# Kernel tuning notes

Hardware: AMD Instinct MI355X
Metric: run time of the kernel (lower is better)

Reference implementation:

```python
import jax, jax.numpy as jnp
import numpy as np

B, S, D, H, E, K, DH = 4, 2048, 1024, 8, 8, 2, 128
ROPE_BASE = 10000.0


def setup_inputs() -> dict:
    key = jax.random.key(0)
    ks = jax.random.split(key, 7)
    s = 1.0 / np.sqrt(D)
    x = jax.random.normal(ks[0], (B, S, D), dtype=jnp.float32)
    Wq = jax.random.normal(ks[1], (H * DH, D), dtype=jnp.float32) * s
    Wk = jax.random.normal(ks[2], (H * DH, D), dtype=jnp.float32) * s
    Wv = jax.random.normal(ks[3], (H * E, D, DH), dtype=jnp.float32) * s
    Wo = jax.random.normal(ks[4], (H * E, DH, D), dtype=jnp.float32) * (1.0 / np.sqrt(H * DH))
    sel_v = jax.random.normal(ks[5], (H * E, D), dtype=jnp.float32) * s
    sel_o = jax.random.normal(ks[6], (H * E, D), dtype=jnp.float32) * s
    positions = jnp.broadcast_to(jnp.arange(S, dtype=jnp.int32), (B, S))
    return {"x": x, "Wq": Wq, "Wk": Wk, "Wv": Wv, "Wo": Wo,
            "sel_v": sel_v, "sel_o": sel_o, "positions": positions}


def _rope(t, pos, inv_freq):
    # t: [b,h,s,d], pos: [b,s]
    freqs = pos.astype(t.dtype)[:, :, None] * inv_freq          # [b,s,d/2]
    emb = jnp.concatenate([freqs, freqs], axis=-1)[:, None]      # [b,1,s,d]
    sin, cos = jnp.sin(emb), jnp.cos(emb)
    x1, x2 = jnp.split(t, 2, axis=-1)
    rot = jnp.concatenate([-x2, x1], axis=-1)
    return t * cos + rot * sin


def reference(x, Wq, Wk, Wv, Wo, sel_v, sel_o, positions):
    # dense shared Q/K projections -> [b,h,s,dh]
    q = (x @ Wq.T).reshape(B, S, H, DH).transpose(0, 2, 1, 3)
    k = (x @ Wk.T).reshape(B, S, H, DH).transpose(0, 2, 1, 3)

    # V expert routing (sigmoid, non-competitive top-k per head)
    gv = jax.nn.sigmoid((x @ sel_v.T).reshape(B, S, H, E))       # [b,s,h,e]
    vw, vi = jax.lax.top_k(gv, K)                                # [b,s,h,k]
    vall = jnp.einsum('bsm,hemd->bshed', x, Wv.reshape(H, E, D, DH))
    vsel = jnp.take_along_axis(vall, vi[..., None], axis=3)      # [b,s,h,k,dh]
    v = (vw[..., None] * vsel).sum(axis=3).transpose(0, 2, 1, 3)  # [b,h,s,dh]

    # RoPE (rotate_fraction=1 -> full head dim)
    inv_freq = 1.0 / (ROPE_BASE ** (jnp.arange(0, DH, 2, dtype=jnp.float32) / DH))
    q = _rope(q, positions, inv_freq)
    k = _rope(k, positions, inv_freq)

    # masked SDPA (causal bool mask, scale 1/sqrt(dh))
    scores = jnp.einsum('bhqd,bhkd->bhqk', q, k) * (1.0 / np.sqrt(DH))
    causal = jnp.tril(jnp.ones((S, S), dtype=bool))
    scores = jnp.where(causal, scores, jnp.finfo(scores.dtype).min)
    attn = jax.nn.softmax(scores, axis=-1)
    ctx = jnp.einsum('bhqk,bhkd->bqhd', attn, v)                  # [b,s,h,dh]

    # O expert routing, combine via scattered gate weights
    go = jax.nn.sigmoid((x @ sel_o.T).reshape(B, S, H, E))
    ow, oi = jax.lax.top_k(go, K)
    g_full = (ow[..., None] * jax.nn.one_hot(oi, E, dtype=x.dtype)).sum(axis=3)  # [b,s,h,e]
    out = jnp.einsum('bshd,bshe,hedm->bsm', ctx, g_full, Wo.reshape(H, E, DH, D))
    return out
```

## Files before the change

### kernel.cpp

```cpp
#include <hip/hip_runtime.h>
#include <math.h>

typedef unsigned short u16;
typedef unsigned int u32;
typedef __attribute__((ext_vector_type(8))) short short8;
typedef __attribute__((ext_vector_type(4))) float f32x4;

constexpr int cB = 4, cS = 2048, cD = 1024, cH = 8, cE = 8, cK = 2, cDH = 128;
constexpr int cBS = cB * cS;
constexpr int cHE = cH * cE;

__device__ inline u16 f2bf(float f) {
    u32 u = __float_as_uint(f);
    u += 0x7fffu + ((u >> 16) & 1u);
    return (u16)(u >> 16);
}
__device__ inline float bf2f(u16 h) { return __uint_as_float(((u32)h) << 16); }

__global__ __launch_bounds__(256) void k_cast_split(
    const float* __restrict__ src, u16* __restrict__ hi, u16* __restrict__ lo)
{
    const size_t i = (size_t)blockIdx.x * 256 + threadIdx.x;
    float4 v = ((const float4*)src)[i];
    u16 hx = f2bf(v.x), hy = f2bf(v.y), hz = f2bf(v.z), hw = f2bf(v.w);
    u16 lx = f2bf(v.x - bf2f(hx)), ly = f2bf(v.y - bf2f(hy));
    u16 lz = f2bf(v.z - bf2f(hz)), lw = f2bf(v.w - bf2f(hw));
    uint2 oh; oh.x = (u32)hx | ((u32)hy << 16); oh.y = (u32)hz | ((u32)hw << 16);
    uint2 ol; ol.x = (u32)lx | ((u32)ly << 16); ol.y = (u32)lz | ((u32)lw << 16);
    ((uint2*)hi)[i] = oh;
    ((uint2*)lo)[i] = ol;
}

__global__ __launch_bounds__(256, 2) void k_gemm_logits3(
    const u16* __restrict__ xh, const u16* __restrict__ xlo,
    const u16* __restrict__ selh, const u16* __restrict__ sell,
    float* __restrict__ lgp)
{
    __shared__ u16 As[128 * 72];
    __shared__ u16 Bs[128 * 72];
    const int r0 = blockIdx.x * 128;
    const int term = blockIdx.y;
    const u16* A = (term == 1) ? xlo : xh;
    const u16* B = (term == 2) ? sell : selh;
    float* outp = lgp + (size_t)term * cBS * 128;
    const int t = threadIdx.x;
    const int w = t >> 6, lane = t & 63;
    const int wm = w >> 1, wn = w & 1;
    const int quad = lane >> 4, lm = lane & 15;

    f32x4 acc[4][4];
#pragma unroll
    for (int i = 0; i < 4; i++)
#pragma unroll
        for (int j = 0; j < 4; j++)
#pragma unroll
            for (int r = 0; r < 4; r++) acc[i][j][r] = 0.0f;

    for (int kc = 0; kc < cD; kc += 64) {
#pragma unroll
        for (int p = 0; p < 4; p++) {
            const int slot = p * 256 + t, row = slot >> 3, seg = slot & 7;
            *(uint4*)(As + row * 72 + seg * 8) =
                *(const uint4*)(A + (size_t)(r0 + row) * cD + kc + seg * 8);
            *(uint4*)(Bs + row * 72 + seg * 8) =
                *(const uint4*)(B + (size_t)row * cD + kc + seg * 8);
        }
        __syncthreads();
#pragma unroll
        for (int ks = 0; ks < 64; ks += 32) {
            short8 av[4], bv[4];
#pragma unroll
            for (int i = 0; i < 4; i++)
                av[i] = *(const short8*)(As + (wm * 64 + i * 16 + lm) * 72 + ks + quad * 8);
#pragma unroll
            for (int j = 0; j < 4; j++)
                bv[j] = *(const short8*)(Bs + (wn * 64 + j * 16 + lm) * 72 + ks + quad * 8);
#pragma unroll
            for (int i = 0; i < 4; i++)
#pragma unroll
                for (int j = 0; j < 4; j++)
                    acc[i][j] = __builtin_amdgcn_mfma_f32_16x16x32_bf16(av[i], bv[j], acc[i][j], 0, 0, 0);
        }
        __syncthreads();
    }
#pragma unroll
    for (int i = 0; i < 4; i++)
#pragma unroll
        for (int r = 0; r < 4; r++) {
            const int row = r0 + wm * 64 + i * 16 + quad * 4 + r;
#pragma unroll
            for (int j = 0; j < 4; j++)
                outp[(size_t)row * 128 + wn * 64 + j * 16 + lm] = acc[i][j][r];
        }
}

__global__ __launch_bounds__(256) void k_top2_flag(
    const float* __restrict__ lgp, float* __restrict__ gv_d, float* __restrict__ go_d,
    int* __restrict__ flags, int* __restrict__ counter)
{
    const int idx = blockIdx.x * 256 + threadIdx.x;
    const int row = idx >> 4, r16 = idx & 15;
    const int which = r16 >> 3, h = r16 & 7;
    const float* l0 = lgp + (size_t)row * 128 + which * 64 + h * 8;
    const float* l1 = l0 + (size_t)cBS * 128;
    const float* l2 = l1 + (size_t)cBS * 128;
    float v[8];
#pragma unroll
    for (int e = 0; e < cE; e++) v[e] = l0[e] + l1[e] + l2[e];
    int i0 = 0; float b0 = v[0];
#pragma unroll
    for (int e = 1; e < cE; e++) { if (v[e] > b0) { b0 = v[e]; i0 = e; } }
    int i1 = -1; float b1 = -3.0e38f;
#pragma unroll
    for (int e = 0; e < cE; e++) { if (e != i0 && v[e] > b1) { b1 = v[e]; i1 = e; } }
    float b2 = -3.0e38f;
#pragma unroll
    for (int e = 0; e < cE; e++) { if (e != i0 && e != i1 && v[e] > b2) b2 = v[e]; }
    const float w0 = 1.0f / (1.0f + __expf(-b0));
    const float w1 = 1.0f / (1.0f + __expf(-b1));
    float* dst = (which ? go_d : gv_d) + (size_t)row * 64 + h * 8;
#pragma unroll
    for (int e = 0; e < cE; e++)
        dst[e] = (e == i0) ? w0 : ((e == i1) ? w1 : 0.0f);
    if (b1 - b2 < 1.0e-3f) {
        const int s = atomicAdd(counter, 1);
        flags[s] = (row << 4) | r16;
    }
}

__global__ __launch_bounds__(64) void k_repair(
    const float* __restrict__ x, const float* __restrict__ sel_v,
    const float* __restrict__ sel_o,
    const int* __restrict__ counter, const int* __restrict__ flags,
    float* __restrict__ gv_d, float* __restrict__ go_d)
{
    const int n = *counter;
    const int lane = threadIdx.x;
    for (int it = blockIdx.x; it < n; it += gridDim.x) {
        const int item = flags[it];
        const int row = item >> 4, which = (item >> 3) & 1, h = item & 7;
        const float* xr = x + (size_t)row * cD;
        const float* sb = (which ? sel_o : sel_v) + (size_t)(h * 8) * cD;
        float lg[8];
#pragma unroll
        for (int e = 0; e < cE; e++) {
            float a = 0.0f;
#pragma unroll
            for (int dg = 0; dg < 4; dg++) {
                const int d = dg * 256 + lane * 4;
                const float4 xv = *(const float4*)(xr + d);
                const float4 sv = *(const float4*)(sb + (size_t)e * cD + d);
                a += xv.x * sv.x + xv.y * sv.y + xv.z * sv.z + xv.w * sv.w;
            }
#pragma unroll
            for (int off = 1; off < 64; off <<= 1) a += __shfl_xor(a, off);
            lg[e] = a;
        }
        int i0 = 0; float b0 = lg[0];
#pragma unroll
        for (int e = 1; e < cE; e++) { if (lg[e] > b0) { b0 = lg[e]; i0 = e; } }
        int i1 = -1; float b1 = -3.0e38f;
#pragma unroll
        for (int e = 0; e < cE; e++) { if (e != i0 && lg[e] > b1) { b1 = lg[e]; i1 = e; } }
        if (lane == 0) {
            const float w0 = 1.0f / (1.0f + expf(-b0));
            const float w1 = 1.0f / (1.0f + expf(-b1));
            float* dst = (which ? go_d : gv_d) + (size_t)row * 64 + h * 8;
#pragma unroll
            for (int e = 0; e < cE; e++)
                dst[e] = (e == i0) ? w0 : ((e == i1) ? w1 : 0.0f);
        }
    }
}

__global__ __launch_bounds__(256) void k_cast_f2b(
    const float* __restrict__ src, u16* __restrict__ dst)
{
    const size_t i = (size_t)blockIdx.x * 256 + threadIdx.x;
    float4 v = ((const float4*)src)[i];
    u32 lo = (u32)f2bf(v.x) | ((u32)f2bf(v.y) << 16);
    u32 hi = (u32)f2bf(v.z) | ((u32)f2bf(v.w) << 16);
    uint2 o; o.x = lo; o.y = hi;
    ((uint2*)dst)[i] = o;
}

__global__ __launch_bounds__(256) void k_cast_wv(
    const float* __restrict__ Wv, u16* __restrict__ WvT)
{
    __shared__ float ld[64][132];
    const int d0 = blockIdx.x * 64, he = blockIdx.y;
    const int t = threadIdx.x;
    for (int p = 0; p < 8; p++) {
        const int slot = p * 256 + t, r = slot >> 5, c4 = slot & 31;
        float4 v = *(const float4*)(Wv + ((size_t)he * cD + d0 + r) * cDH + c4 * 4);
        ld[r][c4 * 4 + 0] = v.x; ld[r][c4 * 4 + 1] = v.y;
        ld[r][c4 * 4 + 2] = v.z; ld[r][c4 * 4 + 3] = v.w;
    }
    __syncthreads();
    for (int p = 0; p < 16; p++) {
        const int slot = p * 256 + t, dh = slot >> 5, c2 = slot & 31;
        u32 val = (u32)f2bf(ld[c2 * 2 + 0][dh]) | ((u32)f2bf(ld[c2 * 2 + 1][dh]) << 16);
        *(u32*)(WvT + (size_t)(he * cDH + dh) * cD + d0 + c2 * 2) = val;
    }
}

__global__ __launch_bounds__(256) void k_cast_wo(
    const float* __restrict__ Wo, u16* __restrict__ WoT)
{
    __shared__ float ld[128][68];
    const int m0 = blockIdx.x * 64, he = blockIdx.y;
    const int t = threadIdx.x;
    for (int p = 0; p < 8; p++) {
        const int slot = p * 256 + t, r = slot >> 4, c4 = slot & 15;
        float4 v = *(const float4*)(Wo + ((size_t)he * cDH + r) * cD + m0 + c4 * 4);
        ld[r][c4 * 4 + 0] = v.x; ld[r][c4 * 4 + 1] = v.y;
        ld[r][c4 * 4 + 2] = v.z; ld[r][c4 * 4 + 3] = v.w;
    }
    __syncthreads();
    for (int p = 0; p < 16; p++) {
        const int slot = p * 256 + t, mr = slot >> 6, c2 = slot & 63;
        u32 val = (u32)f2bf(ld[c2 * 2 + 0][mr]) | ((u32)f2bf(ld[c2 * 2 + 1][mr]) << 16);
        *(u32*)(WoT + (size_t)(m0 + mr) * 8192 + he * cDH + c2 * 2) = val;
    }
}

__global__ __launch_bounds__(256, 2) void k_gemm_v(
    const u16* __restrict__ xh, const u16* __restrict__ WvT,
    const float* __restrict__ gv_d, u16* __restrict__ v_b)
{
    __shared__ u16 As[128 * 72];
    __shared__ u16 Bs[128 * 72];
    __shared__ float Gs[128][9];
    const int rt = blockIdx.x, h = blockIdx.y;
    const int r0 = rt * 128;
    const int t = threadIdx.x;
    const int w = t >> 6, lane = t & 63;
    const int wm = w >> 1, wn = w & 1;
    const int quad = lane >> 4, lm = lane & 15;

    {
        const int row = t >> 1, half = t & 1;
        float4 g4 = *(const float4*)(gv_d + (size_t)(r0 + row) * 64 + h * 8 + half * 4);
        Gs[row][half * 4 + 0] = g4.x; Gs[row][half * 4 + 1] = g4.y;
        Gs[row][half * 4 + 2] = g4.z; Gs[row][half * 4 + 3] = g4.w;
    }

    f32x4 acc[4][4];
#pragma unroll
    for (int i = 0; i < 4; i++)
#pragma unroll
        for (int j = 0; j < 4; j++)
#pragma unroll
            for (int r = 0; r < 4; r++) acc[i][j][r] = 0.0f;

    for (int e = 0; e < cE; e++) {
        f32x4 acce[4][4];
#pragma unroll
        for (int i = 0; i < 4; i++)
#pragma unroll
            for (int j = 0; j < 4; j++)
#pragma unroll
                for (int r = 0; r < 4; r++) acce[i][j][r] = 0.0f;

        for (int kc = 0; kc < cD; kc += 64) {
#pragma unroll
            for (int p = 0; p < 4; p++) {
                const int slot = p * 256 + t, row = slot >> 3, seg = slot & 7;
                *(uint4*)(As + row * 72 + seg * 8) =
                    *(const uint4*)(xh + (size_t)(r0 + row) * cD + kc + seg * 8);
                *(uint4*)(Bs + row * 72 + seg * 8) =
                    *(const uint4*)(WvT + (size_t)((h * 8 + e) * cDH + row) * cD + kc + seg * 8);
            }
            __syncthreads();
#pragma unroll
            for (int ks = 0; ks < 64; ks += 32) {
                short8 av[4], bv[4];
#pragma unroll
                for (int i = 0; i < 4; i++)
                    av[i] = *(const short8*)(As + (wm * 64 + i * 16 + lm) * 72 + ks + quad * 8);
#pragma unroll
                for (int j = 0; j < 4; j++)
                    bv[j] = *(const short8*)(Bs + (wn * 64 + j * 16 + lm) * 72 + ks + quad * 8);
#pragma unroll
                for (int i = 0; i < 4; i++)
#pragma unroll
                    for (int j = 0; j < 4; j++)
                        acce[i][j] = __builtin_amdgcn_mfma_f32_16x16x32_bf16(av[i], bv[j], acce[i][j], 0, 0, 0);
            }
            __syncthreads();
        }
#pragma unroll
        for (int i = 0; i < 4; i++)
#pragma unroll
            for (int r = 0; r < 4; r++) {
                const float g = Gs[wm * 64 + i * 16 + quad * 4 + r][e];
#pragma unroll
                for (int j = 0; j < 4; j++) acc[i][j][r] += g * acce[i][j][r];
            }
    }
#pragma unroll
    for (int i = 0; i < 4; i++)
#pragma unroll
        for (int r = 0; r < 4; r++) {
            const int row = r0 + wm * 64 + i * 16 + quad * 4 + r;
            const int b = row >> 11, s = row & (cS - 1);
            u16* dst = v_b + ((size_t)(b * cH + h) * cS + s) * cDH;
#pragma unroll
            for (int j = 0; j < 4; j++)
                dst[wn * 64 + j * 16 + lm] = f2bf(acc[i][j][r]);
        }
}

__global__ __launch_bounds__(256, 2) void k_gemm_o(
    const u16* __restrict__ ctxh, const u16* __restrict__ WoT,
    const float* __restrict__ go_d, float* __restrict__ out)
{
    __shared__ u16 As[128 * 72];
    __shared__ u16 Bs[128 * 72];
    __shared__ float Gs[128][65];
    const int rt = blockIdx.x, nt = blockIdx.y;
    const int r0 = rt * 128;
    const int t = threadIdx.x;
    const int w = t >> 6, lane = t & 63;
    const int wm = w >> 1, wn = w & 1;
    const int quad = lane >> 4, lm = lane & 15;

#pragma unroll
    for (int p = 0; p < 8; p++) {
        const int slot = p * 256 + t, row = slot >> 4, seg = slot & 15;
        float4 g4 = *(const float4*)(go_d + (size_t)(r0 + row) * 64 + seg * 4);
        Gs[row][seg * 4 + 0] = g4.x; Gs[row][seg * 4 + 1] = g4.y;
        Gs[row][seg * 4 + 2] = g4.z; Gs[row][seg * 4 + 3] = g4.w;
    }

    f32x4 acc[4][4];
#pragma unroll
    for (int i = 0; i < 4; i++)
#pragma unroll
        for (int j = 0; j < 4; j++)
#pragma unroll
            for (int r = 0; r < 4; r++) acc[i][j][r] = 0.0f;

    for (int he = 0; he < cHE; he++) {
        f32x4 acce[4][4];
#pragma unroll
        for (int i = 0; i < 4; i++)
#pragma unroll
            for (int j = 0; j < 4; j++)
#pragma unroll
                for (int r = 0; r < 4; r++) acce[i][j][r] = 0.0f;

#pragma unroll
        for (int kc = 0; kc < 2; kc++) {
            const int ccol = (he >> 3) * 128 + kc * 64;
#pragma unroll
            for (int p = 0; p < 4; p++) {
                const int slot = p * 256 + t, row = slot >> 3, seg = slot & 7;
                *(uint4*)(As + row * 72 + seg * 8) =
                    *(const uint4*)(ctxh + (size_t)(r0 + row) * cD + ccol + seg * 8);
                *(uint4*)(Bs + row * 72 + seg * 8) =
                    *(const uint4*)(WoT + (size_t)(nt * 128 + row) * 8192 + he * 128 + kc * 64 + seg * 8);
            }
            __syncthreads();
#pragma unroll
            for (int ks = 0; ks < 64; ks += 32) {
                short8 av[4], bv[4];
#pragma unroll
                for (int i = 0; i < 4; i++)
                    av[i] = *(const short8*)(As + (wm * 64 + i * 16 + lm) * 72 + ks + quad * 8);
#pragma unroll
                for (int j = 0; j < 4; j++)
                    bv[j] = *(const short8*)(Bs + (wn * 64 + j * 16 + lm) * 72 + ks + quad * 8);
#pragma unroll
                for (int i = 0; i < 4; i++)
#pragma unroll
                    for (int j = 0; j < 4; j++)
                        acce[i][j] = __builtin_amdgcn_mfma_f32_16x16x32_bf16(av[i], bv[j], acce[i][j], 0, 0, 0);
            }
            __syncthreads();
        }
#pragma unroll
        for (int i = 0; i < 4; i++)
#pragma unroll
            for (int r = 0; r < 4; r++) {
                const float g = Gs[wm * 64 + i * 16 + quad * 4 + r][he];
#pragma unroll
                for (int j = 0; j < 4; j++) acc[i][j][r] += g * acce[i][j][r];
            }
    }
#pragma unroll
    for (int i = 0; i < 4; i++)
#pragma unroll
        for (int r = 0; r < 4; r++) {
            const int row = r0 + wm * 64 + i * 16 + quad * 4 + r;
            float* dst = out + (size_t)row * cD + nt * 128;
#pragma unroll
            for (int j = 0; j < 4; j++)
                dst[wn * 64 + j * 16 + lm] = acc[i][j][r];
        }
}

__global__ __launch_bounds__(256, 2) void k_qkproj_mfma(
    const u16* __restrict__ xh, const u16* __restrict__ Wqb,
    const u16* __restrict__ Wkb, float* __restrict__ q_t, float* __restrict__ k_t)
{
    __shared__ u16 As[128 * 72];
    __shared__ u16 Bs[128 * 72];
    const int rt = blockIdx.x, nt = blockIdx.y;
    const bool isK = nt >= cH;
    const int h = isK ? nt - cH : nt;
    const u16* Wb = isK ? Wkb : Wqb;
    float* outp = isK ? k_t : q_t;
    const int r0 = rt * 128;
    const int t = threadIdx.x;
    const int w = t >> 6, lane = t & 63;
    const int wm = w >> 1, wn = w & 1;
    const int quad = lane >> 4, lm = lane & 15;

    f32x4 acc[4][4];
#pragma unroll
    for (int i = 0; i < 4; i++)
#pragma unroll
        for (int j = 0; j < 4; j++)
#pragma unroll
            for (int r = 0; r < 4; r++) acc[i][j][r] = 0.0f;

    for (int kc = 0; kc < cD; kc += 64) {
#pragma unroll
        for (int p = 0; p < 4; p++) {
            const int slot = p * 256 + t, row = slot >> 3, seg = slot & 7;
            *(uint4*)(As + row * 72 + seg * 8) =
                *(const uint4*)(xh + (size_t)(r0 + row) * cD + kc + seg * 8);
            *(uint4*)(Bs + row * 72 + seg * 8) =
                *(const uint4*)(Wb + (size_t)(h * cDH + row) * cD + kc + seg * 8);
        }
        __syncthreads();
#pragma unroll
        for (int ks = 0; ks < 64; ks += 32) {
            short8 av[4], bv[4];
#pragma unroll
            for (int i = 0; i < 4; i++)
                av[i] = *(const short8*)(As + (wm * 64 + i * 16 + lm) * 72 + ks + quad * 8);
#pragma unroll
            for (int j = 0; j < 4; j++)
                bv[j] = *(const short8*)(Bs + (wn * 64 + j * 16 + lm) * 72 + ks + quad * 8);
#pragma unroll
            for (int i = 0; i < 4; i++)
#pragma unroll
                for (int j = 0; j < 4; j++)
                    acc[i][j] = __builtin_amdgcn_mfma_f32_16x16x32_bf16(av[i], bv[j], acc[i][j], 0, 0, 0);
        }
        __syncthreads();
    }
#pragma unroll
    for (int i = 0; i < 4; i++)
#pragma unroll
        for (int r = 0; r < 4; r++) {
            const int row = r0 + wm * 64 + i * 16 + quad * 4 + r;
            const int b = row >> 11, s = row & (cS - 1);
            float* dst = outp + ((size_t)(b * cH + h) * cS + s) * cDH;
#pragma unroll
            for (int j = 0; j < 4; j++)
                dst[wn * 64 + j * 16 + lm] = acc[i][j][r];
        }
}

__global__ __launch_bounds__(256) void k_rope_cast(
    const float* __restrict__ q_t, const float* __restrict__ k_t,
    const int* __restrict__ positions,
    u16* __restrict__ q_b, u16* __restrict__ k_b)
{
    const int total = cB * cH * cS * (cDH / 2);
    const int idx = blockIdx.x * 256 + threadIdx.x;
    const int which = (idx >= total) ? 1 : 0;
    const int id = which ? idx - total : idx;
    const int i = id & 63;
    const int bhs = id >> 6;
    const int s = bhs & (cS - 1);
    const int b = (bhs >> 11) >> 3;
    const float* src = (which ? k_t : q_t) + (size_t)bhs * cDH;
    u16* dst = (which ? k_b : q_b) + (size_t)bhs * cDH;
    const int pos = positions[b * cS + s];
    const float freq = powf(10000.0f, -(float)i / 64.0f);
    const float ang = (float)pos * freq;
    const float c = cosf(ang), sn = sinf(ang);
    const float t1 = src[i], t2 = src[i + 64];
    dst[i] = f2bf(t1 * c - t2 * sn);
    dst[i + 64] = f2bf(t2 * c + t1 * sn);
}

__global__ __launch_bounds__(256, 2) void k_attn_mfma(
    const u16* __restrict__ qb, const u16* __restrict__ kb,
    const u16* __restrict__ vb, u16* __restrict__ ctxh)
{
    __shared__ u16 Ks[64][136];
    __shared__ u16 VsT[128][72];
    __shared__ u16 Ps[4][32][72];

    const int combined = blockIdx.z * 8 + blockIdx.y;
    const int qtv = (combined < 16) ? (15 - (int)blockIdx.x) : (int)blockIdx.x;
    const int h = blockIdx.y, b = blockIdx.z;
    const int q0 = qtv * 128;
    const int t = threadIdx.x;
    const int w = t >> 6, lane = t & 63;
    const int quad = lane >> 4, lm = lane & 15;
    const size_t bh = (size_t)(b * cH + h) * cS;
    const u16* kbase = kb + bh * cDH;
    const u16* vbase = vb + bh * cDH;

    short8 aq[2][4];
#pragma unroll
    for (int mi = 0; mi < 2; mi++) {
        const u16* qrow = qb + (bh + q0 + w * 32 + mi * 16 + lm) * cDH;
#pragma unroll
        for (int ks = 0; ks < 4; ks++)
            aq[mi][ks] = *(const short8*)(qrow + ks * 32 + quad * 8);
    }

    f32x4 o_acc[2][8];
#pragma unroll
    for (int mi = 0; mi < 2; mi++)
#pragma unroll
        for (int j = 0; j < 8; j++)
#pragma unroll
            for (int r = 0; r < 4; r++) o_acc[mi][j][r] = 0.0f;
    float m_r[2][4], l_r[2][4];
#pragma unroll
    for (int mi = 0; mi < 2; mi++)
#pragma unroll
        for (int r = 0; r < 4; r++) { m_r[mi][r] = -1.0e30f; l_r[mi][r] = 0.0f; }
    const float scale = 0.08838834764831845f;
    const int nkt = 2 * qtv + 2;

    for (int kt = 0; kt < nkt; kt++) {
        const int k0 = kt * 64;
#pragma unroll
        for (int p = 0; p < 4; p++) {
            const int slot = p * 256 + t, row = slot >> 4, seg = slot & 15;
            *(uint4*)&Ks[row][seg * 8] =
                *(const uint4*)(kbase + (size_t)(k0 + row) * cDH + seg * 8);
        }
        {
            const int rq = t & 15, seg = t >> 4;
            uint4 r0v = *(const uint4*)(vbase + (size_t)(k0 + rq * 4 + 0) * cDH + seg * 8);
            uint4 r1v = *(const uint4*)(vbase + (size_t)(k0 + rq * 4 + 1) * cDH + seg * 8);
            uint4 r2v = *(const uint4*)(vbase + (size_t)(k0 + rq * 4 + 2) * cDH + seg * 8);
            uint4 r3v = *(const uint4*)(vbase + (size_t)(k0 + rq * 4 + 3) * cDH + seg * 8);
            const u16* p0 = (const u16*)&r0v; const u16* p1 = (const u16*)&r1v;
            const u16* p2 = (const u16*)&r2v; const u16* p3 = (const u16*)&r3v;
#pragma unroll
            for (int jj = 0; jj < 8; jj++) {
                ushort4 val;
                val.x = p0[jj]; val.y = p1[jj]; val.z = p2[jj]; val.w = p3[jj];
                *(ushort4*)&VsT[seg * 8 + jj][rq * 4] = val;
            }
        }
        __syncthreads();

        f32x4 s[2][4];
#pragma unroll
        for (int mi = 0; mi < 2; mi++)
#pragma unroll
            for (int j = 0; j < 4; j++)
#pragma unroll
                for (int r = 0; r < 4; r++) s[mi][j][r] = 0.0f;
#pragma unroll
        for (int ks = 0; ks < 4; ks++) {
#pragma unroll
            for (int j = 0; j < 4; j++) {
                short8 bv = *(const short8*)&Ks[j * 16 + lm][ks * 32 + quad * 8];
                s[0][j] = __builtin_amdgcn_mfma_f32_16x16x32_bf16(aq[0][ks], bv, s[0][j], 0, 0, 0);
                s[1][j] = __builtin_amdgcn_mfma_f32_16x16x32_bf16(aq[1][ks], bv, s[1][j], 0, 0, 0);
            }
        }
        if (kt >= nkt - 2) {
#pragma unroll
            for (int mi = 0; mi < 2; mi++)
#pragma unroll
                for (int j = 0; j < 4; j++) {
                    const int colg = k0 + j * 16 + lm;
#pragma unroll
                    for (int r = 0; r < 4; r++) {
                        const int rowg = q0 + w * 32 + mi * 16 + quad * 4 + r;
                        s[mi][j][r] = (colg <= rowg) ? s[mi][j][r] * scale : -1.0e30f;
                    }
                }
        } else {
#pragma unroll
            for (int mi = 0; mi < 2; mi++)
#pragma unroll
                for (int j = 0; j < 4; j++)
#pragma unroll
                    for (int r = 0; r < 4; r++) s[mi][j][r] *= scale;
        }
#pragma unroll
        for (int mi = 0; mi < 2; mi++) {
            float mt[4];
#pragma unroll
            for (int r = 0; r < 4; r++)
                mt[r] = fmaxf(fmaxf(s[mi][0][r], s[mi][1][r]), fmaxf(s[mi][2][r], s[mi][3][r]));
#pragma unroll
            for (int off = 1; off < 16; off <<= 1)
#pragma unroll
                for (int r = 0; r < 4; r++) mt[r] = fmaxf(mt[r], __shfl_xor(mt[r], off));
            float alpha[4], rs[4];
#pragma unroll
            for (int r = 0; r < 4; r++) {
                const float mn = fmaxf(m_r[mi][r], mt[r]);
                alpha[r] = __expf(m_r[mi][r] - mn);
                m_r[mi][r] = mn;
                rs[r] = 0.0f;
            }
#pragma unroll
            for (int j = 0; j < 4; j++)
#pragma unroll
                for (int r = 0; r < 4; r++) {
                    const float p = __expf(s[mi][j][r] - m_r[mi][r]);
                    s[mi][j][r] = p;
                    rs[r] += p;
                }
#pragma unroll
            for (int off = 1; off < 16; off <<= 1)
#pragma unroll
                for (int r = 0; r < 4; r++) rs[r] += __shfl_xor(rs[r], off);
#pragma unroll
            for (int r = 0; r < 4; r++) l_r[mi][r] = l_r[mi][r] * alpha[r] + rs[r];
#pragma unroll
            for (int j = 0; j < 8; j++)
#pragma unroll
                for (int r = 0; r < 4; r++) o_acc[mi][j][r] *= alpha[r];
#pragma unroll
            for (int j = 0; j < 4; j++)
#pragma unroll
                for (int r = 0; r < 4; r++)
                    Ps[w][mi * 16 + quad * 4 + r][j * 16 + lm] = f2bf(s[mi][j][r]);
        }
#pragma unroll
        for (int ks2 = 0; ks2 < 2; ks2++) {
            short8 ap0 = *(const short8*)&Ps[w][lm][ks2 * 32 + quad * 8];
            short8 ap1 = *(const short8*)&Ps[w][16 + lm][ks2 * 32 + quad * 8];
#pragma unroll
            for (int j2 = 0; j2 < 8; j2++) {
                short8 bv = *(const short8*)&VsT[j2 * 16 + lm][ks2 * 32 + quad * 8];
                o_acc[0][j2] = __builtin_amdgcn_mfma_f32_16x16x32_bf16(ap0, bv, o_acc[0][j2], 0, 0, 0);
                o_acc[1][j2] = __builtin_amdgcn_mfma_f32_16x16x32_bf16(ap1, bv, o_acc[1][j2], 0, 0, 0);
            }
        }
        __syncthreads();
    }
#pragma unroll
    for (int mi = 0; mi < 2; mi++)
#pragma unroll
        for (int r = 0; r < 4; r++) {
            const float inv = 1.0f / l_r[mi][r];
            const int sg = q0 + w * 32 + mi * 16 + quad * 4 + r;
            u16* dst = ctxh + (((size_t)b * cS + sg) * cH + h) * cDH;
#pragma unroll
            for (int j2 = 0; j2 < 8; j2++)
                dst[j2 * 16 + lm] = f2bf(o_acc[mi][j2][r] * inv);
        }
}

extern "C" void kernel_launch(void* const* d_in, const int* in_sizes, int n_in,
                              void* d_out, int out_size, void* d_ws, size_t ws_size,
                              hipStream_t stream)
{
    const float* x = (const float*)d_in[0];
    const float* Wq = (const float*)d_in[1];
    const float* Wk = (const float*)d_in[2];
    const float* Wv = (const float*)d_in[3];
    const float* Wo = (const float*)d_in[4];
    const float* sel_v = (const float*)d_in[5];
    const float* sel_o = (const float*)d_in[6];
    const int* positions = (const int*)d_in[7];
    float* out = (float*)d_out;

    char* ws = (char*)d_ws;
    size_t off = 0;
    auto alloc = [&](size_t bytes) -> void* {
        void* p = ws + off;
        off += (bytes + 255) & ~(size_t)255;
        return p;
    };
    const size_t big = (size_t)cB * cH * cS * cDH * sizeof(float);
    const size_t half = big / 2;
    char* R1 = (char*)alloc(big);
    char* R2 = (char*)alloc(big);
    char* R3 = (char*)alloc(big);
    char* R4 = (char*)alloc(big);
    float* gv_d = (float*)alloc((size_t)cBS * 64 * sizeof(float));
    float* go_d = (float*)alloc((size_t)cBS * 64 * sizeof(float));
    u16* selh = (u16*)alloc((size_t)128 * cD * sizeof(u16));
    u16* sell = (u16*)alloc((size_t)128 * cD * sizeof(u16));
    int* flags = (int*)alloc((size_t)cBS * 16 * sizeof(int));
    int* counter = (int*)alloc(256);

    u16* WvT = (u16*)R1;
    float* lgp = (float*)(R1 + half);
    float* q_t = (float*)R1;
    u16* xlo = (u16*)R2;
    float* k_t = (float*)R2;
    u16* WoT = (u16*)R2;
    u16* v_b = (u16*)R3;
    u16* Wqb = (u16*)(R3 + half);
    u16* Wkb = (u16*)(R3 + half + ((size_t)cD * cD * 2));
    u16* ctxh = (u16*)(R3 + half);
    u16* xh = (u16*)R4;
    u16* q_b = (u16*)R4;
    u16* k_b = (u16*)(R4 + half);

    hipMemsetAsync(counter, 0, sizeof(int), stream);

    k_cast_split<<<8192, 256, 0, stream>>>(x, xh, xlo);
    k_cast_split<<<64, 256, 0, stream>>>(sel_v, selh, sell);
    k_cast_split<<<64, 256, 0, stream>>>(sel_o, selh + (size_t)cHE * cD,
                                         sell + (size_t)cHE * cD);
    k_gemm_logits3<<<dim3(64, 3), 256, 0, stream>>>(xh, xlo, selh, sell, lgp);
    k_top2_flag<<<512, 256, 0, stream>>>(lgp, gv_d, go_d, flags, counter);
    k_repair<<<256, 64, 0, stream>>>(x, sel_v, sel_o, counter, flags, gv_d, go_d);

    k_cast_wv<<<dim3(16, 64), 256, 0, stream>>>(Wv, WvT);
    k_gemm_v<<<dim3(64, 8), 256, 0, stream>>>(xh, WvT, gv_d, v_b);

    k_cast_f2b<<<1024, 256, 0, stream>>>(Wq, Wqb);
    k_cast_f2b<<<1024, 256, 0, stream>>>(Wk, Wkb);
    k_qkproj_mfma<<<dim3(64, 16), 256, 0, stream>>>(xh, Wqb, Wkb, q_t, k_t);
    k_rope_cast<<<(2 * cB * cH * cS * (cDH / 2)) / 256, 256, 0, stream>>>(
        q_t, k_t, positions, q_b, k_b);
    k_attn_mfma<<<dim3(16, 8, 4), 256, 0, stream>>>(q_b, k_b, v_b, ctxh);

    k_cast_wo<<<dim3(16, 64), 256, 0, stream>>>(Wo, WoT);
    k_gemm_o<<<dim3(64, 8), 256, 0, stream>>>(ctxh, WoT, go_d, out);
}
```

Baseline: 739.6 us.

## Route V projection through per-expert gathered token lists instead of dense all-expert GEMM

Builds per (head, slot, expert) token lists with atomics, then runs grouped GEMMs that compute only the two selected experts per token instead of all eight. This cuts V-projection MFMA work by about four times. The cost is gathered row loads, an fp32 partial buffer written in the first pass and read back in the second, and list-building overhead. RoPE now also uses exp2f and __sincosf in place of powf/sinf/cosf, which is cheaper but less precise for large angles.

```diff
diff --git a/kernel.cpp b/kernel.cpp
--- a/kernel.cpp
+++ b/kernel.cpp
@@ -9,6 +9,7 @@
 constexpr int cB = 4, cS = 2048, cD = 1024, cH = 8, cE = 8, cK = 2, cDH = 128;
 constexpr int cBS = cB * cS;
 constexpr int cHE = cH * cE;
+constexpr int cCAP = 8192;
 
 __device__ inline u16 f2bf(float f) {
     u32 u = __float_as_uint(f);
@@ -173,6 +174,27 @@
     }
 }
 
+__global__ __launch_bounds__(256) void k_build_lists(
+    const float* __restrict__ gv_d, int* __restrict__ cnt,
+    int* __restrict__ idxb, float* __restrict__ gateb)
+{
+    const int idx = blockIdx.x * 256 + threadIdx.x;
+    const int row = idx >> 3, h = idx & 7;
+    const float* g = gv_d + (size_t)row * 64 + h * 8;
+    int e0 = 0; float w0 = g[0];
+#pragma unroll
+    for (int e = 1; e < cE; e++) { const float ge = g[e]; if (ge > w0) { w0 = ge; e0 = e; } }
+    int e1 = -1; float w1 = -1.0f;
+#pragma unroll
+    for (int e = 0; e < cE; e++) { const float ge = g[e]; if (e != e0 && ge > w1) { w1 = ge; e1 = e; } }
+    const int g0 = (h * 2 + 0) * 8 + e0;
+    const int p0 = atomicAdd(&cnt[g0], 1);
+    idxb[g0 * cCAP + p0] = row; gateb[g0 * cCAP + p0] = w0;
+    const int g1 = (h * 2 + 1) * 8 + e1;
+    const int p1 = atomicAdd(&cnt[g1], 1);
+    idxb[g1 * cCAP + p1] = row; gateb[g1 * cCAP + p1] = w1;
+}
+
 __global__ __launch_bounds__(256) void k_cast_f2b(
     const float* __restrict__ src, u16* __restrict__ dst)
 {
@@ -224,26 +246,40 @@
     }
 }
 
-__global__ __launch_bounds__(256, 2) void k_gemm_v(
+template<int SLOT>
+__global__ __launch_bounds__(256, 2) void k_gemm_v_grp(
     const u16* __restrict__ xh, const u16* __restrict__ WvT,
-    const float* __restrict__ gv_d, u16* __restrict__ v_b)
+    const int* __restrict__ cnt, const int* __restrict__ idxb,
+    const float* __restrict__ gateb,
+    float* __restrict__ vp, u16* __restrict__ v_b)
 {
     __shared__ u16 As[128 * 72];
     __shared__ u16 Bs[128 * 72];
-    __shared__ float Gs[128][9];
-    const int rt = blockIdx.x, h = blockIdx.y;
-    const int r0 = rt * 128;
+    __shared__ int Ridx[128];
+    __shared__ float Gts[128];
+    const int h = blockIdx.x >> 3, e = blockIdx.x & 7;
+    const int grp = (h * 2 + SLOT) * 8 + e;
+    const int n = cnt[grp];
+    const int tile = blockIdx.y;
+    if (tile * 128 >= n) return;
+    const int m = min(128, n - tile * 128);
     const int t = threadIdx.x;
     const int w = t >> 6, lane = t & 63;
     const int wm = w >> 1, wn = w & 1;
     const int quad = lane >> 4, lm = lane & 15;
 
-    {
-        const int row = t >> 1, half = t & 1;
-        float4 g4 = *(const float4*)(gv_d + (size_t)(r0 + row) * 64 + h * 8 + half * 4);
-        Gs[row][half * 4 + 0] = g4.x; Gs[row][half * 4 + 1] = g4.y;
-        Gs[row][half * 4 + 2] = g4.z; Gs[row][half * 4 + 3] = g4.w;
-    }
+    if (t < 128) {
+        const int base = grp * cCAP + tile * 128;
+        Ridx[t] = (t < m) ? idxb[base + t] : idxb[base];
+        Gts[t] = (t < m) ? gateb[base + t] : 0.0f;
+    }
+    __syncthreads();
+
+    const int srow = t >> 3, seg = t & 7;
+    int arow[4];
+#pragma unroll
+    for (int p = 0; p < 4; p++) arow[p] = Ridx[p * 32 + srow];
+    const u16* Bbase = WvT + (size_t)((h * 8 + e) * cDH) * cD;
 
     f32x4 acc[4][4];
 #pragma unroll
@@ -253,61 +289,55 @@
 #pragma unroll
             for (int r = 0; r < 4; r++) acc[i][j][r] = 0.0f;
 
-    for (int e = 0; e < cE; e++) {
-        f32x4 acce[4][4];
-#pragma unroll
-        for (int i = 0; i < 4; i++)
-#pragma unroll
-            for (int j = 0; j < 4; j++)
-#pragma unroll
-                for (int r = 0; r < 4; r++) acce[i][j][r] = 0.0f;
-
-        for (int kc = 0; kc < cD; kc += 64) {
-#pragma unroll
-            for (int p = 0; p < 4; p++) {
-                const int slot = p * 256 + t, row = slot >> 3, seg = slot & 7;
-                *(uint4*)(As + row * 72 + seg * 8) =
-                    *(const uint4*)(xh + (size_t)(r0 + row) * cD + kc + seg * 8);
-                *(uint4*)(Bs + row * 72 + seg * 8) =
-                    *(const uint4*)(WvT + (size_t)((h * 8 + e) * cDH + row) * cD + kc + seg * 8);
-            }
-            __syncthreads();
-#pragma unroll
-            for (int ks = 0; ks < 64; ks += 32) {
-                short8 av[4], bv[4];
-#pragma unroll
-                for (int i = 0; i < 4; i++)
-                    av[i] = *(const short8*)(As + (wm * 64 + i * 16 + lm) * 72 + ks + quad * 8);
+    for (int kc = 0; kc < cD; kc += 64) {
+#pragma unroll
+        for (int p = 0; p < 4; p++) {
+            const int row = p * 32 + srow;
+            *(uint4*)(As + row * 72 + seg * 8) =
+                *(const uint4*)(xh + (size_t)arow[p] * cD + kc + seg * 8);
+            *(uint4*)(Bs + row * 72 + seg * 8) =
+                *(const uint4*)(Bbase + (size_t)row * cD + kc + seg * 8);
+        }
+        __syncthreads();
+#pragma unroll
+        for (int ks = 0; ks < 64; ks += 32) {
+            short8 av[4], bv[4];
+#pragma unroll
+            for (int i = 0; i < 4; i++)
+                av[i] = *(const short8*)(As + (wm * 64 + i * 16 + lm) * 72 + ks + quad * 8);
+#pragma unroll
+            for (int j = 0; j < 4; j++)
+                bv[j] = *(const short8*)(Bs + (wn * 64 + j * 16 + lm) * 72 + ks + quad * 8);
+#pragma unroll
+            for (int i = 0; i < 4; i++)
 #pragma unroll
                 for (int j = 0; j < 4; j++)
-                    bv[j] = *(const short8*)(Bs + (wn * 64 + j * 16 + lm) * 72 + ks + quad * 8);
-#pragma unroll
-                for (int i = 0; i < 4; i++)
+                    acc[i][j] = __builtin_amdgcn_mfma_f32_16x16x32_bf16(av[i], bv[j], acc[i][j], 0, 0, 0);
+        }
+        __syncthreads();
+    }
+#pragma unroll
+    for (int i = 0; i < 4; i++)
+#pragma unroll
+        for (int r = 0; r < 4; r++) {
+            const int ti = wm * 64 + i * 16 + quad * 4 + r;
+            if (ti < m) {
+                const int row = Ridx[ti];
+                const float gt = Gts[ti];
+                const int b = row >> 11, s = row & (cS - 1);
+                const size_t base = ((size_t)(b * cH + h) * cS + s) * cDH;
+                if (SLOT == 0) {
 #pragma unroll
                     for (int j = 0; j < 4; j++)
-                        acce[i][j] = __builtin_amdgcn_mfma_f32_16x16x32_bf16(av[i], bv[j], acce[i][j], 0, 0, 0);
-            }
-            __syncthreads();
-        }
-#pragma unroll
-        for (int i = 0; i < 4; i++)
-#pragma unroll
-            for (int r = 0; r < 4; r++) {
-                const float g = Gs[wm * 64 + i * 16 + quad * 4 + r][e];
-#pragma unroll
-                for (int j = 0; j < 4; j++) acc[i][j][r] += g * acce[i][j][r];
-            }
-    }
-#pragma unroll
-    for (int i = 0; i < 4; i++)
-#pragma unroll
-        for (int r = 0; r < 4; r++) {
-            const int row = r0 + wm * 64 + i * 16 + quad * 4 + r;
-            const int b = row >> 11, s = row & (cS - 1);
-            u16* dst = v_b + ((size_t)(b * cH + h) * cS + s) * cDH;
-#pragma unroll
-            for (int j = 0; j < 4; j++)
-                dst[wn * 64 + j * 16 + lm] = f2bf(acc[i][j][r]);
+                        vp[base + wn * 64 + j * 16 + lm] = gt * acc[i][j][r];
+                } else {
+#pragma unroll
+                    for (int j = 0; j < 4; j++) {
+                        const int col = wn * 64 + j * 16 + lm;
+                        v_b[base + col] = f2bf(gt * acc[i][j][r] + vp[base + col]);
+                    }
+                }
+            }
         }
 }
 
@@ -481,9 +511,10 @@
     const float* src = (which ? k_t : q_t) + (size_t)bhs * cDH;
     u16* dst = (which ? k_b : q_b) + (size_t)bhs * cDH;
     const int pos = positions[b * cS + s];
-    const float freq = powf(10000.0f, -(float)i / 64.0f);
+    const float freq = exp2f((float)i * -0.20762050593745932f);
     const float ang = (float)pos * freq;
-    const float c = cosf(ang), sn = sinf(ang);
+    float sn, c;
+    __sincosf(ang, &sn, &c);
     const float t1 = src[i], t2 = src[i + 64];
     dst[i] = f2bf(t1 * c - t2 * sn);
     dst[i + 64] = f2bf(t2 * c + t1 * sn);
@@ -694,11 +725,15 @@
     u16* sell = (u16*)alloc((size_t)128 * cD * sizeof(u16));
     int* flags = (int*)alloc((size_t)cBS * 16 * sizeof(int));
     int* counter = (int*)alloc(256);
+    int* cntv = (int*)alloc(512);
+    int* idxv = (int*)alloc((size_t)128 * cCAP * sizeof(int));
+    float* gatev = (float*)alloc((size_t)128 * cCAP * sizeof(float));
 
     u16* WvT = (u16*)R1;
     float* lgp = (float*)(R1 + half);
     float* q_t = (float*)R1;
     u16* xlo = (u16*)R2;
+    float* vp = (float*)R2;
     float* k_t = (float*)R2;
     u16* WoT = (u16*)R2;
     u16* v_b = (u16*)R3;
@@ -710,6 +745,7 @@
     u16* k_b = (u16*)(R4 + half);
 
     hipMemsetAsync(counter, 0, sizeof(int), stream);
+    hipMemsetAsync(cntv, 0, 128 * sizeof(int), stream);
 
     k_cast_split<<<8192, 256, 0, stream>>>(x, xh, xlo);
     k_cast_split<<<64, 256, 0, stream>>>(sel_v, selh, sell);
@@ -719,8 +755,10 @@
     k_top2_flag<<<512, 256, 0, stream>>>(lgp, gv_d, go_d, flags, counter);
     k_repair<<<256, 64, 0, stream>>>(x, sel_v, sel_o, counter, flags, gv_d, go_d);
 
+    k_build_lists<<<256, 256, 0, stream>>>(gv_d, cntv, idxv, gatev);
     k_cast_wv<<<dim3(16, 64), 256, 0, stream>>>(Wv, WvT);
-    k_gemm_v<<<dim3(64, 8), 256, 0, stream>>>(xh, WvT, gv_d, v_b);
+    k_gemm_v_grp<0><<<dim3(64, 64), 256, 0, stream>>>(xh, WvT, cntv, idxv, gatev, vp, v_b);
+    k_gemm_v_grp<1><<<dim3(64, 64), 256, 0, stream>>>(xh, WvT, cntv, idxv, gatev, vp, v_b);
 
     k_cast_f2b<<<1024, 256, 0, stream>>>(Wq, Wqb);
     k_cast_f2b<<<1024, 256, 0, stream>>>(Wk, Wkb);
```

New measurement: 822.0 us. +11.2%, slower.
